# Optimization experiments

Hardware: AMD Instinct MI355X
Metric: run time of the kernel (lower is better)

## Reference

```python
import jax, jax.numpy as jnp
import numpy as np

DK, DV, NH = 512, 256, 8  # matches init_kwargs


def rel_to_abs(x):
    # x: (B, N, L, 2L-1) -> (B, N, L, L) via pad/reshape trick
    B, N, L, _ = x.shape
    x = jnp.pad(x, ((0, 0), (0, 0), (0, 0), (0, 1)))          # (B,N,L,2L)
    x = x.reshape(B, N, L * 2 * L)
    x = jnp.pad(x, ((0, 0), (0, 0), (0, L - 1)))
    x = x.reshape(B, N, L + 1, 2 * L - 1)
    return x[:, :, :L, L - 1:]


def relative_logits_1d(q, rel_k):
    # q: (B, nh, A, Wd, dkh); rel_k: (dkh, 2*Wd-1)
    B, nh, A, Wd, _ = q.shape
    rel = jnp.einsum('bnawc,cm->bnawm', q, rel_k)             # (B,nh,A,Wd,2Wd-1)
    rel = rel.reshape(B, nh * A, Wd, 2 * Wd - 1)
    rel = rel_to_abs(rel).reshape(B, nh, A, 1, Wd, Wd)
    return jnp.broadcast_to(rel, (B, nh, A, A, Wd, Wd))


def reference(x, w_qkv, w_conv, w_out, key_rel_h, key_rel_w):
    B, Cin, H, W = x.shape
    dkh, dvh = DK // NH, DV // NH
    L = H * W
    # 1x1 qkv projection (stride 1)
    qkv = jnp.einsum('bchw,oc->bohw', x, w_qkv)               # (B, 2dk+dv, H, W)
    q = qkv[:, :DK]
    k = qkv[:, DK:2 * DK]
    v = qkv[:, 2 * DK:]
    flat_q = q.reshape(B, NH, dkh, L) * (dkh ** -0.5)
    flat_k = k.reshape(B, NH, dkh, L)
    flat_v = v.reshape(B, NH, dvh, L)
    logits = jnp.einsum('bncs,bnct->bnst', flat_q, flat_k)     # (B,nh,L,L)
    # relative position logits (uses the already-scaled q, as in the torch code)
    qr = flat_q.reshape(B, NH, dkh, H, W).transpose(0, 1, 3, 4, 2)  # (B,nh,H,W,dkh)
    w_rel = relative_logits_1d(qr, key_rel_w)                  # (B,nh,H,H,W,W)
    h_rel = relative_logits_1d(qr.transpose(0, 1, 3, 2, 4), key_rel_h)  # (B,nh,W,W,H,H)
    h_rel = h_rel.transpose(0, 1, 2, 4, 3, 5).reshape(B, NH, L, L)
    w_rel = w_rel.transpose(0, 1, 4, 2, 5, 3).reshape(B, NH, L, L)
    logits = logits + h_rel + w_rel
    weights = jax.nn.softmax(logits, axis=-1)
    attn = jnp.einsum('bnst,bnct->bnsc', weights, flat_v)      # (B,nh,L,dvh)
    attn = attn.transpose(0, 1, 3, 2).reshape(B, DV, H, W)
    attn = jnp.einsum('bchw,oc->bohw', attn, w_out)            # 1x1 out_proj
    conv_out = jax.lax.conv_general_dilated(
        x, w_conv, window_strides=(1, 1), padding=[(1, 1), (1, 1)],
        dimension_numbers=('NCHW', 'OIHW', 'NCHW'))            # (B, out_c-dv, H, W)
    return jnp.concatenate([conv_out, attn], axis=1)


def setup_inputs() -> dict:
    key = jax.random.key(0)
    ks = jax.random.split(key, 6)
    H, W, Cin = 32, 32, 256
    return {
        'x': jax.random.normal(ks[0], (8, Cin, H, W), jnp.float32),
        'w_qkv': jax.random.normal(ks[1], (2 * DK + DV, Cin), jnp.float32) * 0.02,
        'w_conv': jax.random.normal(ks[2], (256, Cin, 3, 3), jnp.float32) * 0.02,
        'w_out': jax.random.normal(ks[3], (DV, DV), jnp.float32) * 0.02,
        'key_rel_h': DK ** -0.5 + jax.random.normal(ks[4], (DK // NH, 2 * H - 1), jnp.float32),
        'key_rel_w': DK ** -0.5 + jax.random.normal(ks[5], (DK // NH, 2 * W - 1), jnp.float32),
    }
```

## Files before the change

### kernel.cpp

```cpp
#include <hip/hip_runtime.h>
#include <cstddef>
#include <cstdint>

#define NB 8
#define CIN 256
#define LL 1024
#define DKC 512
#define DVC 256
#define XPSTRIDE 295936

typedef short short8 __attribute__((ext_vector_type(8)));
typedef float f32x4 __attribute__((ext_vector_type(4)));

typedef __attribute__((address_space(1))) const unsigned int gas_u32;
typedef __attribute__((address_space(3))) unsigned int las_u32;

__device__ __forceinline__ unsigned short f2bf(float f) {
  unsigned int u = __float_as_uint(f);
  u += 0x7fffu + ((u >> 16) & 1u);
  return (unsigned short)(u >> 16);
}
__device__ __forceinline__ float bf2f(unsigned short u) {
  return __uint_as_float(((unsigned int)u) << 16);
}

__global__ __launch_bounds__(256) void prep_all(
    const float* __restrict__ x, const float* __restrict__ wconv,
    const float* __restrict__ wqkv, const float* __restrict__ wout,
    const float* __restrict__ krh, const float* __restrict__ krw,
    unsigned short* __restrict__ xTp, unsigned short* __restrict__ wtap,
    unsigned short* __restrict__ wqbf, unsigned short* __restrict__ woutbf,
    unsigned short* __restrict__ relTh, unsigned short* __restrict__ relTw) {
  __shared__ float tile[64][65];
  const int bx = blockIdx.x;
  const int tid = threadIdx.x;
  if (bx < 128) {
    const int st = bx & 15;
    const int b = bx >> 4;
    const int s0 = st * 64;
    const int h0 = st * 2;
    for (int cc = 0; cc < 4; ++cc) {
      const int c0 = cc * 64;
      {
        const int row = tid >> 2;
        const int j0 = (tid & 3) * 16;
#pragma unroll
        for (int k = 0; k < 4; ++k)
          *(float4*)&tile[row][j0 + k * 4] =
              *(const float4*)(x + ((size_t)(b * CIN + c0 + row)) * LL + s0 + j0 + k * 4);
      }
      __syncthreads();
      {
        const int sl = tid >> 2;
        const int cb = (tid & 3) * 16;
        unsigned short buf[16];
#pragma unroll
        for (int m = 0; m < 16; ++m) buf[m] = f2bf(tile[cb + m][sl]);
        const int hp = h0 + (sl >> 5) + 1;
        const int wp = (sl & 31) + 1;
        unsigned short* dst = xTp + (size_t)b * XPSTRIDE + (hp * 34 + wp) * 256 + c0 + cb;
        *(uint4*)dst = *(uint4*)&buf[0];
        *(uint4*)(dst + 8) = *(uint4*)&buf[8];
      }
      __syncthreads();
    }
  } else if (bx < 1184) {
    const int idx = (bx - 128) * 256 + tid;
    const int b = idx / 33792;
    const int rem = idx - b * 33792;
    const int pos = rem >> 8, c = rem & 255;
    int hp, wp;
    if (pos < 34) { hp = 0; wp = pos; }
    else if (pos < 68) { hp = 33; wp = pos - 34; }
    else if (pos < 100) { hp = pos - 68 + 1; wp = 0; }
    else { hp = pos - 100 + 1; wp = 33; }
    xTp[(size_t)b * XPSTRIDE + (hp * 34 + wp) * 256 + c] = 0;
  } else {
    const int idx = (bx - 1184) * 256 + tid;
    if (idx < 589824) {
      const int tap = idx >> 16;
      const int rem = idx & 65535;
      wtap[idx] = f2bf(wconv[(size_t)rem * 9 + tap]);
    } else if (idx < 917504) {
      const int j = idx - 589824;
      const int o = j >> 8;
      const float sc = (o < DKC) ? 0.125f * 1.44269504088896f : 1.0f;
      wqbf[j] = f2bf(wqkv[j] * sc);
    } else if (idx < 983040) {
      const int j = idx - 917504;
      woutbf[j] = f2bf(wout[j]);
    } else {
      const int j = idx - 983040;
      const int tbl = j >> 12;
      const int rest = j & 4095;
      const int m = rest >> 6, c = rest & 63;
      const float* src = tbl ? krw : krh;
      unsigned short* dst = tbl ? relTw : relTh;
      const float v = (m < 63) ? src[c * 63 + m] : 0.f;
      dst[m * 64 + c] = f2bf(v);
    }
  }
}

__global__ __launch_bounds__(256) void qkvconv_mfma(
    const unsigned short* __restrict__ xTp, const unsigned short* __restrict__ wqbf,
    const unsigned short* __restrict__ wtap, unsigned short* __restrict__ qbf,
    unsigned short* __restrict__ kbf, unsigned short* __restrict__ vbf,
    float* __restrict__ out) {
  __shared__ __align__(16) char smem[32768];
  const int tid = threadIdx.x;
  const int lane = tid & 63, w = tid >> 6;
  const int n16 = lane & 15, quad = lane >> 4;
  const int lin = blockIdx.x;
  const int trow = tid >> 3;
  const int ck = tid & 7;
  const int lr = lane >> 3;
  const int lg = lane & 7;
  const int gsw = (lg ^ lr) * 8;

  if (lin < 512) {
    const int ot = lin & 3;
    const int st = (lin >> 2) & 15;
    const int b = lin >> 6;
    const int s0 = st * 64;
    const int h0 = st * 2;
    unsigned short* asb = (unsigned short*)smem;
    unsigned short* bsb = (unsigned short*)(smem + 16384);
    const unsigned short* xb = xTp + (size_t)b * XPSTRIDE;
    const unsigned short* wbase = wtap + (size_t)(ot * 64) * 256;

    f32x4 acc[4];
#pragma unroll
    for (int nt = 0; nt < 4; ++nt) acc[nt] = (f32x4){0.f, 0.f, 0.f, 0.f};

    auto issue = [&](int it, int bufi) {
      const int tap = it >> 2;
      const int c0 = (it & 3) * 64;
      const int dh = tap / 3 - 1;
      const int dw = tap - (tap / 3) * 3 - 1;
      const unsigned short* wt = wbase + (size_t)tap * 65536;
      unsigned short* ad = asb + bufi * 4096 + w * 512;
      unsigned short* bd = bsb + bufi * 4096 + w * 512;
      const unsigned short* asrc = wt + (size_t)trow * 256 + c0 + gsw;
      __builtin_amdgcn_global_load_lds((gas_u32*)asrc, (las_u32*)ad, 16, 0, 0);
      __builtin_amdgcn_global_load_lds((gas_u32*)(asrc + 32 * 256), (las_u32*)(ad + 2048), 16, 0, 0);
      const int wp = trow + dw + 1;
      const unsigned short* bsrc = xb + (size_t)((h0 + dh + 1) * 34 + wp) * 256 + c0 + gsw;
      __builtin_amdgcn_global_load_lds((gas_u32*)bsrc, (las_u32*)bd, 16, 0, 0);
      __builtin_amdgcn_global_load_lds((gas_u32*)(bsrc + 34 * 256), (las_u32*)(bd + 2048), 16, 0, 0);
    };
    issue(0, 0);
    for (int it = 0; it < 36; ++it) {
      __syncthreads();
      if (it < 35) issue(it + 1, (it + 1) & 1);
      const unsigned short* ab = asb + (it & 1) * 4096;
      const unsigned short* bb = bsb + (it & 1) * 4096;
      short8 a0 = *(const short8*)&ab[(w * 16 + n16) * 64 + ((quad ^ (n16 & 7)) * 8)];
      short8 a1 = *(const short8*)&ab[(w * 16 + n16) * 64 + (((quad + 4) ^ (n16 & 7)) * 8)];
#pragma unroll
      for (int nt = 0; nt < 4; ++nt) {
        short8 b0 = *(const short8*)&bb[(nt * 16 + n16) * 64 + ((quad ^ (n16 & 7)) * 8)];
        short8 b1 = *(const short8*)&bb[(nt * 16 + n16) * 64 + (((quad + 4) ^ (n16 & 7)) * 8)];
        acc[nt] = __builtin_amdgcn_mfma_f32_16x16x32_bf16(a0, b0, acc[nt], 0, 0, 0);
        acc[nt] = __builtin_amdgcn_mfma_f32_16x16x32_bf16(a1, b1, acc[nt], 0, 0, 0);
      }
    }
#pragma unroll
    for (int nt = 0; nt < 4; ++nt)
#pragma unroll
      for (int reg = 0; reg < 4; ++reg)
        out[((size_t)b * 512 + ot * 64 + w * 16 + quad * 4 + reg) * LL + s0 + nt * 16 + n16] =
            acc[nt][reg];
  } else {
    const int l2 = lin - 512;
    const int ot = l2 % 20;
    const int rest = l2 / 20;
    const int st = rest & 15;
    const int b = rest >> 4;
    const int o0 = ot * 64;
    const int s0 = st * 64;
    const int h0 = st * 2;
    unsigned short* asb = (unsigned short*)smem;
    unsigned short* bsb = (unsigned short*)(smem + 16384);
    float (*trans)[65] = (float(*)[65])smem;

    const unsigned short* xb = xTp + (size_t)b * XPSTRIDE;
    const unsigned short* wt = wqbf + (size_t)o0 * 256;

    f32x4 acc[4];
#pragma unroll
    for (int nt = 0; nt < 4; ++nt) acc[nt] = (f32x4){0.f, 0.f, 0.f, 0.f};

    auto issue = [&](int kc, int bufi) {
      const int c0 = kc * 64;
      unsigned short* ad = asb + bufi * 4096 + w * 512;
      unsigned short* bd = bsb + bufi * 4096 + w * 512;
      const unsigned short* asrc = wt + (size_t)trow * 256 + c0 + gsw;
      __builtin_amdgcn_global_load_lds((gas_u32*)asrc, (las_u32*)ad, 16, 0, 0);
      __builtin_amdgcn_global_load_lds((gas_u32*)(asrc + 32 * 256), (las_u32*)(ad + 2048), 16, 0, 0);
      const int wpos = trow + 1;
      const unsigned short* bsrc = xb + (size_t)((h0 + 1) * 34 + wpos) * 256 + c0 + gsw;
      __builtin_amdgcn_global_load_lds((gas_u32*)bsrc, (las_u32*)bd, 16, 0, 0);
      __builtin_amdgcn_global_load_lds((gas_u32*)(bsrc + 34 * 256), (las_u32*)(bd + 2048), 16, 0, 0);
    };
    issue(0, 0);
#pragma unroll
    for (int kc = 0; kc < 4; ++kc) {
      __syncthreads();
      if (kc < 3) issue(kc + 1, (kc + 1) & 1);
      const unsigned short* as = asb + (kc & 1) * 4096;
      const unsigned short* bs = bsb + (kc & 1) * 4096;
      short8 a0 = *(const short8*)&as[(w * 16 + n16) * 64 + ((quad ^ (n16 & 7)) * 8)];
      short8 a1 = *(const short8*)&as[(w * 16 + n16) * 64 + (((quad + 4) ^ (n16 & 7)) * 8)];
#pragma unroll
      for (int nt = 0; nt < 4; ++nt) {
        short8 b0 = *(const short8*)&bs[(nt * 16 + n16) * 64 + ((quad ^ (n16 & 7)) * 8)];
        short8 b1 = *(const short8*)&bs[(nt * 16 + n16) * 64 + (((quad + 4) ^ (n16 & 7)) * 8)];
        acc[nt] = __builtin_amdgcn_mfma_f32_16x16x32_bf16(a0, b0, acc[nt], 0, 0, 0);
        acc[nt] = __builtin_amdgcn_mfma_f32_16x16x32_bf16(a1, b1, acc[nt], 0, 0, 0);
      }
    }
    __syncthreads();
#pragma unroll
    for (int nt = 0; nt < 4; ++nt)
#pragma unroll
      for (int reg = 0; reg < 4; ++reg)
        trans[w * 16 + quad * 4 + reg][nt * 16 + n16] = acc[nt][reg];
    __syncthreads();
    const int sl = tid >> 2;
    const int cseg = (tid & 3) * 16;
    unsigned short buf[16];
    if (ot < 16) {
#pragma unroll
      for (int m = 0; m < 16; ++m) buf[m] = f2bf(trans[cseg + m][sl]);
      unsigned short* dst;
      int head;
      if (ot < 8) { dst = qbf; head = ot; }
      else { dst = kbf; head = ot - 8; }
      const size_t base = (((size_t)(b * 8 + head)) * LL + s0 + sl) * 64 + cseg;
      *(uint4*)(dst + base) = *(uint4*)&buf[0];
      *(uint4*)(dst + base + 8) = *(uint4*)&buf[8];
    } else {
#pragma unroll
      for (int m = 0; m < 16; ++m) buf[m] = f2bf(trans[sl][cseg + m]);
      unsigned short* dst = vbf + ((size_t)b * DVC + (ot - 16) * 64 + sl) * LL + s0 + cseg;
      *(uint4*)dst = *(uint4*)&buf[0];
      *(uint4*)(dst + 8) = *(uint4*)&buf[8];
    }
  }
}

__global__ __launch_bounds__(256, 4) void attn_kernel(
    const unsigned short* __restrict__ qbf, const unsigned short* __restrict__ kbf,
    const unsigned short* __restrict__ vbf, const unsigned short* __restrict__ relTh,
    const unsigned short* __restrict__ relTw, unsigned short* __restrict__ abf) {
  __shared__ __align__(16) char smem[32768];
  unsigned short* ks = (unsigned short*)smem;
  unsigned short* vs = (unsigned short*)(smem + 16384);
  unsigned short* rwtT = (unsigned short*)(smem + 24576);
  unsigned short* ps = (unsigned short*)(smem + 8192);
  float* obuf = (float*)smem;

  const int tid = threadIdx.x;
  const int lane = tid & 63, w = tid >> 6;
  const int n16 = lane & 15, quad = lane >> 4;
  const int blk = blockIdx.x;
  const int bn = blk & 63, qb = blk >> 6;
  const int n = bn & 7, b = bn >> 3;
  const int s0 = qb * 64;
  const int aa = 2 * qb + (w >> 1);
  const int pb = (w & 1) * 16;

  const unsigned short* qbase = qbf + ((size_t)(b * 8 + n)) * LL * 64;
  const unsigned short* kbase = kbf + ((size_t)(b * 8 + n)) * LL * 64;
  const unsigned short* vbase = vbf + ((size_t)(b * 8 + n)) * 32 * LL;

  const int lr = lane >> 3;
  const int lg = lane & 7;
  const int wkey = (lr & 3) | ((w & 1) << 2);
  const int gsw = (lg ^ wkey) * 8;
  const int krow0 = w * 8 + lr;
  const int krb = (n16 >> 2) * 8 + (n16 & 3);
  const int kk = (n16 & 3) | (((n16 >> 2) & 1) << 2);
  const int vk = (n16 & 3) | (((n16 >> 3) & 1) << 2);
  const int qcol = w * 16 + n16;

  auto issue_tile = [&](int t0, int bufi) {
    unsigned short* kd = ks + bufi * 4096 + w * 512;
    unsigned short* vd = vs + bufi * 2048 + w * 512;
    const unsigned short* ksrc = kbase + (size_t)(t0 + krow0) * 64 + gsw;
    __builtin_amdgcn_global_load_lds((gas_u32*)ksrc, (las_u32*)kd, 16, 0, 0);
    __builtin_amdgcn_global_load_lds((gas_u32*)(ksrc + 32 * 64), (las_u32*)(kd + 2048), 16, 0, 0);
    __builtin_amdgcn_global_load_lds((gas_u32*)(vbase + (size_t)krow0 * LL + t0 + gsw),
                                     (las_u32*)vd, 16, 0, 0);
  };

  issue_tile(0, 0);

  {
    const int sT = (pb + n16) * 32 + aa;
    short8 ra0 = *(const short8*)(qbase + (size_t)sT * 64 + quad * 8);
    short8 ra1 = *(const short8*)(qbase + (size_t)sT * 64 + 32 + quad * 8);
#pragma unroll
    for (int tbl = 0; tbl < 2; ++tbl) {
      const unsigned short* rel = tbl ? relTh : relTw;
      f32x4 acc[4];
#pragma unroll
      for (int mt = 0; mt < 4; ++mt) acc[mt] = (f32x4){0.f, 0.f, 0.f, 0.f};
#pragma unroll
      for (int mt = 0; mt < 4; ++mt) {
        short8 b0 = *(const short8*)(rel + (mt * 16 + n16) * 64 + quad * 8);
        short8 b1 = *(const short8*)(rel + (mt * 16 + n16) * 64 + 32 + quad * 8);
        acc[mt] = __builtin_amdgcn_mfma_f32_16x16x32_bf16(ra0, b0, acc[mt], 0, 0, 0);
        acc[mt] = __builtin_amdgcn_mfma_f32_16x16x32_bf16(ra1, b1, acc[mt], 0, 0, 0);
      }
      if (tbl == 0) {
#pragma unroll
        for (int mt = 0; mt < 4; ++mt)
#pragma unroll
          for (int reg = 0; reg < 4; ++reg)
            rwtT[(mt * 16 + n16) * 64 +
                 ((w * 16 + quad * 4 + reg) ^ ((n16 & 7) * 8))] = f2bf(acc[mt][reg]);
      } else {
#pragma unroll
        for (int mt = 0; mt < 4; ++mt)
#pragma unroll
          for (int reg = 0; reg < 4; ++reg)
            ps[(w * 16 + quad * 4 + reg) * 64 + mt * 16 + n16] = f2bf(acc[mt][reg]);
      }
    }
  }
  short8 qf0 = *(const short8*)(qbase + (size_t)(s0 + w * 16 + n16) * 64 + quad * 8);
  short8 qf1 = *(const short8*)(qbase + (size_t)(s0 + w * 16 + n16) * 64 + 32 + quad * 8);
  __syncthreads();
  float rhreg[2][4];
#pragma unroll
  for (int c1 = 0; c1 < 2; ++c1)
#pragma unroll
    for (int reg = 0; reg < 4; ++reg)
      rhreg[c1][reg] =
          bf2f(ps[qcol * 64 + quad * 8 + c1 * 4 + reg + 31 - pb - n16]);
  __syncthreads();

  float lacc[4] = {0.f, 0.f, 0.f, 0.f};
  f32x4 oacc[2];
  oacc[0] = (f32x4){0.f, 0.f, 0.f, 0.f};
  oacc[1] = (f32x4){0.f, 0.f, 0.f, 0.f};

  int cur = 0;
  for (int kt64 = 0; kt64 < 16; ++kt64) {
    const int t0 = kt64 * 64;
    __syncthreads();
    if (kt64 < 15) issue_tile(t0 + 64, cur ^ 1);
    const unsigned short* ksb = ks + cur * 4096;
    const unsigned short* vsb = vs + cur * 2048;

    f32x4 sacc[4];
#pragma unroll
    for (int c = 0; c < 4; ++c) sacc[c] = (f32x4){0.f, 0.f, 0.f, 0.f};
#pragma unroll
    for (int c = 0; c < 4; ++c) {
      const int ro = (krb + (c & 1) * 4 + (c >> 1) * 32) * 64;
      short8 kb0 = *(const short8*)&ksb[ro + ((quad ^ kk) * 8)];
      short8 kb1 = *(const short8*)&ksb[ro + (((quad + 4) ^ kk) * 8)];
      sacc[c] = __builtin_amdgcn_mfma_f32_16x16x32_bf16(kb0, qf0, sacc[c], 0, 0, 0);
      sacc[c] = __builtin_amdgcn_mfma_f32_16x16x32_bf16(kb1, qf1, sacc[c], 0, 0, 0);
    }
    float rww[2];
#pragma unroll
    for (int h = 0; h < 2; ++h) {
      const int mw = (t0 >> 5) + h - aa + 31;
      rww[h] = bf2f(rwtT[mw * 64 + (qcol ^ ((mw & 7) * 8))]);
    }
    unsigned int pkw[2][4];
#pragma unroll
    for (int c = 0; c < 4; ++c) {
      float e[4];
#pragma unroll
      for (int reg = 0; reg < 4; ++reg) {
        e[reg] = __builtin_amdgcn_exp2f(sacc[c][reg] + rww[c >> 1] + rhreg[c & 1][reg]);
        lacc[reg] += e[reg];
      }
      unsigned int p0, p1;
      asm("v_cvt_pk_bf16_f32 %0, %1, %2" : "=v"(p0) : "v"(e[0]), "v"(e[1]));
      asm("v_cvt_pk_bf16_f32 %0, %1, %2" : "=v"(p1) : "v"(e[2]), "v"(e[3]));
      pkw[c >> 1][(c & 1) * 2] = p0;
      pkw[c >> 1][(c & 1) * 2 + 1] = p1;
    }
#pragma unroll
    for (int kt = 0; kt < 2; ++kt) {
      uint4 pw;
      pw.x = pkw[kt][0]; pw.y = pkw[kt][1]; pw.z = pkw[kt][2]; pw.w = pkw[kt][3];
      short8 pa = *(short8*)&pw;
#pragma unroll
      for (int ct = 0; ct < 2; ++ct) {
        short8 vb = *(const short8*)&vsb[(ct * 16 + n16) * 64 + (((quad + 4 * kt) ^ vk) * 8)];
        oacc[ct] = __builtin_amdgcn_mfma_f32_16x16x32_bf16(pa, vb, oacc[ct], 0, 0, 0);
      }
    }
    cur ^= 1;
  }
  float lsum = (lacc[0] + lacc[1]) + (lacc[2] + lacc[3]);
  lsum += __shfl_xor(lsum, 16);
  lsum += __shfl_xor(lsum, 32);
  const float linv_own = 1.0f / lsum;
  float linv[4];
#pragma unroll
  for (int reg = 0; reg < 4; ++reg)
    linv[reg] = __shfl(linv_own, (lane & 48) | (quad * 4 + reg));
  __syncthreads();
#pragma unroll
  for (int ct = 0; ct < 2; ++ct)
#pragma unroll
    for (int reg = 0; reg < 4; ++reg)
      obuf[(w * 16 + quad * 4 + reg) * 33 + ct * 16 + n16] = oacc[ct][reg] * linv[reg];
  __syncthreads();
  {
    const int row = tid >> 2;
    const int cseg = (tid & 3) * 8;
    unsigned short buf8[8];
#pragma unroll
    for (int m = 0; m < 8; ++m) buf8[m] = f2bf(obuf[row * 33 + cseg + m]);
    *(uint4*)(abf + (((size_t)b * LL) + s0 + row) * 256 + n * 32 + cseg) = *(uint4*)&buf8[0];
  }
}

__global__ __launch_bounds__(256) void proj_mfma(
    const unsigned short* __restrict__ abf, const unsigned short* __restrict__ woutbf,
    float* __restrict__ out) {
  __shared__ __align__(16) unsigned short as[64 * 64];
  __shared__ __align__(16) unsigned short bs[64 * 64];
  const int tid = threadIdx.x;
  const int lane = tid & 63, w = tid >> 6;
  const int n16 = lane & 15, quad = lane >> 4;
  const int ot = blockIdx.x;
  const int st = blockIdx.y;
  const int b = blockIdx.z;
  const int o0 = ot * 64;
  const int s0 = st * 64;
  const int trow = tid >> 3, ck = tid & 7;

  const unsigned short* ab = abf + ((size_t)b * LL + s0) * 256;
  const unsigned short* wt = woutbf + (size_t)o0 * 256;

  f32x4 acc[4];
#pragma unroll
  for (int nt = 0; nt < 4; ++nt) acc[nt] = (f32x4){0.f, 0.f, 0.f, 0.f};

  uint4 ra0, ra1, rb0, rb1;
  ra0 = *(const uint4*)(wt + (size_t)trow * 256 + ck * 8);
  ra1 = *(const uint4*)(wt + (size_t)(trow + 32) * 256 + ck * 8);
  rb0 = *(const uint4*)(ab + (size_t)trow * 256 + ck * 8);
  rb1 = *(const uint4*)(ab + (size_t)(trow + 32) * 256 + ck * 8);
#pragma unroll
  for (int kc = 0; kc < 4; ++kc) {
    __syncthreads();
    *(uint4*)&as[trow * 64 + ((ck ^ (trow & 7)) * 8)] = ra0;
    *(uint4*)&as[(trow + 32) * 64 + ((ck ^ (trow & 7)) * 8)] = ra1;
    *(uint4*)&bs[trow * 64 + ((ck ^ (trow & 7)) * 8)] = rb0;
    *(uint4*)&bs[(trow + 32) * 64 + ((ck ^ (trow & 7)) * 8)] = rb1;
    __syncthreads();
    if (kc < 3) {
      const int c0 = (kc + 1) * 64;
      ra0 = *(const uint4*)(wt + (size_t)trow * 256 + c0 + ck * 8);
      ra1 = *(const uint4*)(wt + (size_t)(trow + 32) * 256 + c0 + ck * 8);
      rb0 = *(const uint4*)(ab + (size_t)trow * 256 + c0 + ck * 8);
      rb1 = *(const uint4*)(ab + (size_t)(trow + 32) * 256 + c0 + ck * 8);
    }
    short8 a0 = *(const short8*)&as[(w * 16 + n16) * 64 + ((quad ^ (n16 & 7)) * 8)];
    short8 a1 = *(const short8*)&as[(w * 16 + n16) * 64 + (((quad + 4) ^ (n16 & 7)) * 8)];
#pragma unroll
    for (int nt = 0; nt < 4; ++nt) {
      short8 b0 = *(const short8*)&bs[(nt * 16 + n16) * 64 + ((quad ^ (n16 & 7)) * 8)];
      short8 b1 = *(const short8*)&bs[(nt * 16 + n16) * 64 + (((quad + 4) ^ (n16 & 7)) * 8)];
      acc[nt] = __builtin_amdgcn_mfma_f32_16x16x32_bf16(a0, b0, acc[nt], 0, 0, 0);
      acc[nt] = __builtin_amdgcn_mfma_f32_16x16x32_bf16(a1, b1, acc[nt], 0, 0, 0);
    }
  }
#pragma unroll
  for (int nt = 0; nt < 4; ++nt)
#pragma unroll
    for (int reg = 0; reg < 4; ++reg)
      out[((size_t)b * 512 + 256 + o0 + w * 16 + quad * 4 + reg) * LL + s0 + nt * 16 + n16] =
          acc[nt][reg];
}

extern "C" void kernel_launch(void* const* d_in, const int* in_sizes, int n_in,
                              void* d_out, int out_size, void* d_ws, size_t ws_size,
                              hipStream_t stream) {
  const float* x     = (const float*)d_in[0];
  const float* wqkv  = (const float*)d_in[1];
  const float* wconv = (const float*)d_in[2];
  const float* wout  = (const float*)d_in[3];
  const float* krh   = (const float*)d_in[4];
  const float* krw   = (const float*)d_in[5];
  float* out = (float*)d_out;

  unsigned short* qbf = (unsigned short*)d_ws;
  unsigned short* kbf = qbf + (size_t)NB * 8 * LL * 64;
  unsigned short* vbf = kbf + (size_t)NB * 8 * LL * 64;
  unsigned short* abf = vbf + (size_t)NB * DVC * LL;
  unsigned short* relTh = abf + (size_t)NB * LL * DVC;
  unsigned short* relTw = relTh + 4096;
  unsigned short* xTp = relTw + 4096;
  unsigned short* wtap = xTp + (size_t)NB * XPSTRIDE;
  unsigned short* wqbf = wtap + 589824;
  unsigned short* woutbf = wqbf + 327680;

  prep_all<<<dim3(5056), 256, 0, stream>>>(x, wconv, wqkv, wout, krh, krw,
                                           xTp, wtap, wqbf, woutbf, relTh, relTw);
  qkvconv_mfma<<<dim3(3072), 256, 0, stream>>>(xTp, wqbf, wtap, qbf, kbf, vbf, out);
  attn_kernel<<<dim3(1024), 256, 0, stream>>>(qbf, kbf, vbf, relTh, relTw, abf);
  proj_mfma<<<dim3(4, 16, NB), 256, 0, stream>>>(abf, woutbf, out);
}
```

Before: 137.4 us.

## Double-buffer out-projection tiles via direct global-to-LDS loads; coalesce conv-weight reads

```diff
diff --git a/kernel.cpp b/kernel.cpp
--- a/kernel.cpp
+++ b/kernel.cpp
@@ -78,9 +78,10 @@
   } else {
     const int idx = (bx - 1184) * 256 + tid;
     if (idx < 589824) {
-      const int tap = idx >> 16;
-      const int rem = idx & 65535;
-      wtap[idx] = f2bf(wconv[(size_t)rem * 9 + tap]);
+      const int j = idx;
+      const int rem = j / 9;
+      const int tap = j - rem * 9;
+      wtap[tap * 65536 + rem] = f2bf(wconv[j]);
     } else if (idx < 917504) {
       const int j = idx - 589824;
       const int o = j >> 8;
@@ -428,8 +429,9 @@
 __global__ __launch_bounds__(256) void proj_mfma(
     const unsigned short* __restrict__ abf, const unsigned short* __restrict__ woutbf,
     float* __restrict__ out) {
-  __shared__ __align__(16) unsigned short as[64 * 64];
-  __shared__ __align__(16) unsigned short bs[64 * 64];
+  __shared__ __align__(16) char smem[32768];
+  unsigned short* asb = (unsigned short*)smem;
+  unsigned short* bsb = (unsigned short*)(smem + 16384);
   const int tid = threadIdx.x;
   const int lane = tid & 63, w = tid >> 6;
   const int n16 = lane & 15, quad = lane >> 4;
@@ -438,7 +440,10 @@
   const int b = blockIdx.z;
   const int o0 = ot * 64;
   const int s0 = st * 64;
-  const int trow = tid >> 3, ck = tid & 7;
+  const int trow = tid >> 3;
+  const int lr = lane >> 3;
+  const int lg = lane & 7;
+  const int gsw = (lg ^ lr) * 8;
 
   const unsigned short* ab = abf + ((size_t)b * LL + s0) * 256;
   const unsigned short* wt = woutbf + (size_t)o0 * 256;
@@ -447,26 +452,24 @@
 #pragma unroll
   for (int nt = 0; nt < 4; ++nt) acc[nt] = (f32x4){0.f, 0.f, 0.f, 0.f};
 
-  uint4 ra0, ra1, rb0, rb1;
-  ra0 = *(const uint4*)(wt + (size_t)trow * 256 + ck * 8);
-  ra1 = *(const uint4*)(wt + (size_t)(trow + 32) * 256 + ck * 8);
-  rb0 = *(const uint4*)(ab + (size_t)trow * 256 + ck * 8);
-  rb1 = *(const uint4*)(ab + (size_t)(trow + 32) * 256 + ck * 8);
+  auto issue = [&](int kc, int bufi) {
+    const int c0 = kc * 64;
+    unsigned short* ad = asb + bufi * 4096 + w * 512;
+    unsigned short* bd = bsb + bufi * 4096 + w * 512;
+    const unsigned short* asrc = wt + (size_t)trow * 256 + c0 + gsw;
+    __builtin_amdgcn_global_load_lds((gas_u32*)asrc, (las_u32*)ad, 16, 0, 0);
+    __builtin_amdgcn_global_load_lds((gas_u32*)(asrc + 32 * 256), (las_u32*)(ad + 2048), 16, 0, 0);
+    const unsigned short* bsrc = ab + (size_t)trow * 256 + c0 + gsw;
+    __builtin_amdgcn_global_load_lds((gas_u32*)bsrc, (las_u32*)bd, 16, 0, 0);
+    __builtin_amdgcn_global_load_lds((gas_u32*)(bsrc + 32 * 256), (las_u32*)(bd + 2048), 16, 0, 0);
+  };
+  issue(0, 0);
 #pragma unroll
   for (int kc = 0; kc < 4; ++kc) {
     __syncthreads();
-    *(uint4*)&as[trow * 64 + ((ck ^ (trow & 7)) * 8)] = ra0;
-    *(uint4*)&as[(trow + 32) * 64 + ((ck ^ (trow & 7)) * 8)] = ra1;
-    *(uint4*)&bs[trow * 64 + ((ck ^ (trow & 7)) * 8)] = rb0;
-    *(uint4*)&bs[(trow + 32) * 64 + ((ck ^ (trow & 7)) * 8)] = rb1;
-    __syncthreads();
-    if (kc < 3) {
-      const int c0 = (kc + 1) * 64;
-      ra0 = *(const uint4*)(wt + (size_t)trow * 256 + c0 + ck * 8);
-      ra1 = *(const uint4*)(wt + (size_t)(trow + 32) * 256 + c0 + ck * 8);
-      rb0 = *(const uint4*)(ab + (size_t)trow * 256 + c0 + ck * 8);
-      rb1 = *(const uint4*)(ab + (size_t)(trow + 32) * 256 + c0 + ck * 8);
-    }
+    if (kc < 3) issue(kc + 1, (kc + 1) & 1);
+    const unsigned short* as = asb + (kc & 1) * 4096;
+    const unsigned short* bs = bsb + (kc & 1) * 4096;
     short8 a0 = *(const short8*)&as[(w * 16 + n16) * 64 + ((quad ^ (n16 & 7)) * 8)];
     short8 a1 = *(const short8*)&as[(w * 16 + n16) * 64 + (((quad + 4) ^ (n16 & 7)) * 8)];
 #pragma unroll
```

Measured after the change: 138.8 us. Within noise of the previous version (+1.0%).
